# Performance work log

Measured on AMD Instinct MI355X. Metric: run time of the kernel, lower is better.

Reference implementation:

```python
import jax, jax.numpy as jnp
import numpy as np


def setup_inputs() -> dict:
    key = jax.random.key(0)
    ks = jax.random.split(key, 8)
    B, N, D, H = 8, 512, 64, 64
    user_embeddings = jax.random.normal(ks[0], (B, N, D), dtype=jnp.float32)
    past_lengths = jax.random.randint(ks[1], (B,), 0, N)
    valid_mask = jnp.ones((B, N), dtype=jnp.float32)
    # MLP params: Linear(4D -> H), PReLU (single slope), Linear(H -> 1)
    s1 = 1.0 / np.sqrt(4 * D)
    s2 = 1.0 / np.sqrt(H)
    W1 = jax.random.uniform(ks[2], (H, 4 * D), minval=-s1, maxval=s1, dtype=jnp.float32)
    b1 = jax.random.uniform(ks[3], (H,), minval=-s1, maxval=s1, dtype=jnp.float32)
    prelu_a = jnp.float32(0.25)
    W2 = jax.random.uniform(ks[4], (1, H), minval=-s2, maxval=s2, dtype=jnp.float32)
    b2 = jax.random.uniform(ks[5], (1,), minval=-s2, maxval=s2, dtype=jnp.float32)
    return {"past_lengths": past_lengths, "user_embeddings": user_embeddings,
            "valid_mask": valid_mask, "W1": W1, "b1": b1, "prelu_a": prelu_a,
            "W2": W2, "b2": b2}


def reference(past_lengths, user_embeddings, valid_mask, W1, b1, prelu_a, W2, b2):
    # DIN local activation attention with causal mask.
    # Original math: h = W1 @ concat(Q, K, Q-K, Q*K) + b1 per (q,k) pair.
    # Split W1 into its 4 D-sized blocks so the concat tensor [B,N,N,4D] is
    # never materialized; the pairwise hidden [B,N,N,H] is the only big buffer.
    B, N, D = user_embeddings.shape
    Wq, Wk, Wd, Wm = jnp.split(W1, 4, axis=1)  # each [H, D]
    x = user_embeddings
    # Q and (Q-K)'s +Q part -> per-query term; K and (Q-K)'s -K part -> per-key term
    hq = jnp.einsum('bqd,hd->bqh', x, Wq + Wd)          # [B,N,H]
    hk = jnp.einsum('bkd,hd->bkh', x, Wk - Wd)          # [B,N,H]
    hm = jnp.einsum('bqd,bkd,hd->bqkh', x, x, Wm)       # [B,N,N,H] (Q*K term)
    h = hq[:, :, None, :] + hk[:, None, :, :] + hm + b1
    h = jnp.where(h > 0, h, prelu_a * h)                # PReLU
    scores = jnp.einsum('bqkh,h->bqk', h, W2[0]) + b2[0]  # [B,N,N]
    causal = jnp.tril(jnp.ones((N, N), dtype=scores.dtype))
    scores = scores * causal[None, :, :]
    scores = scores * valid_mask[:, None, :]            # key-side padding mask
    encoded = jnp.einsum('bqk,bkd->bqd', scores, x)     # weighted sum (no softmax)
    return encoded
```

## Files before the change

kernel.cpp:

```cpp
#include <hip/hip_runtime.h>

#define NB 8
#define NN 512

#define WS_WMF 0
#define WS_HQ  4096
#define WS_BF  266240
#define WS_XE  528384

typedef float fx4 __attribute__((ext_vector_type(4)));
typedef short sx8 __attribute__((ext_vector_type(8)));
typedef int   ix4 __attribute__((ext_vector_type(4)));

static __device__ inline unsigned short f2bf(float f) {
    unsigned u = __float_as_uint(f);
    return (unsigned short)((u + 0x7FFFu + ((u >> 16) & 1u)) >> 16);
}

__global__ __launch_bounds__(256) void prep(const float* __restrict__ x,
                                            const float* __restrict__ vm,
                                            const float* __restrict__ W1,
                                            const float* __restrict__ b1,
                                            float* __restrict__ ws) {
    __shared__ float lwq[64 * 68];
    __shared__ float lwk[64 * 68];
    __shared__ float xs[256];
    const int t = threadIdx.x;
    const int blk = blockIdx.x;

    {
        int d = t & 63, hb = t >> 6;
        #pragma unroll 4
        for (int i = 0; i < 16; ++i) {
            int h = i * 4 + hb;
            float a = W1[h * 256 + d];
            float bb = W1[h * 256 + 64 + d];
            float c = W1[h * 256 + 128 + d];
            lwq[h * 68 + d] = a + c;
            lwk[h * 68 + d] = bb - c;
        }
    }
    const int r0 = blk * 4;
    xs[t] = x[r0 * 64 + t];
    __syncthreads();

    {
        int r = t >> 6, h = t & 63;
        const fx4* xr  = (const fx4*)(xs + r * 64);
        const fx4* wqv = (const fx4*)(lwq + h * 68);
        const fx4* wkv = (const fx4*)(lwk + h * 68);
        float aq = b1[h], ak = 0.f;
        #pragma unroll
        for (int dd = 0; dd < 16; ++dd) {
            fx4 xv = xr[dd];
            fx4 wq = wqv[dd];
            fx4 wk = wkv[dd];
            aq = fmaf(xv[0], wq[0], aq); aq = fmaf(xv[1], wq[1], aq);
            aq = fmaf(xv[2], wq[2], aq); aq = fmaf(xv[3], wq[3], aq);
            ak = fmaf(xv[0], wk[0], ak); ak = fmaf(xv[1], wk[1], ak);
            ak = fmaf(xv[2], wk[2], ak); ak = fmaf(xv[3], wk[3], ak);
        }
        int row = r0 + r;
        (ws + WS_HQ)[row * 64 + h] = aq;
        unsigned short* bfp = (unsigned short*)(ws + WS_BF);
        int bb = row >> 9, k = row & 511;
        int tt = k >> 4, nn = k & 15;
        int c = 2 + (h >> 5);
        int qd = (h >> 3) & 3, j = h & 7;
        int ln = qd * 16 + nn;
        bfp[((((bb * 32 + tt) * 4 + c) * 64 + ln) << 3) + j] = f2bf(ak);
    }

    if (blk < 256) {
        int b = blk >> 5, t5 = blk & 31;
        if (t < 128) {
            unsigned short* bfp = (unsigned short*)(ws + WS_BF);
            int c = t >> 6, L = t & 63;
            int nn = L & 15, qd = L >> 4;
            const float* src = x + ((b * 512 + t5 * 16 + nn) * 64 + c * 32 + qd * 8);
            fx4 v0 = *(const fx4*)src;
            fx4 v1 = *(const fx4*)(src + 4);
            uint4 o;
            o.x = (unsigned)f2bf(v0[0]) | ((unsigned)f2bf(v0[1]) << 16);
            o.y = (unsigned)f2bf(v0[2]) | ((unsigned)f2bf(v0[3]) << 16);
            o.z = (unsigned)f2bf(v1[0]) | ((unsigned)f2bf(v1[1]) << 16);
            o.w = (unsigned)f2bf(v1[2]) | ((unsigned)f2bf(v1[3]) << 16);
            *(uint4*)(bfp + ((((b * 32 + t5) * 4 + c) * 64 + L) << 3)) = o;
        }
        {
            unsigned short* xep = (unsigned short*)(ws + WS_XE);
            int c32 = t5 >> 1, half = t5 & 1;
            int nt = t >> 6, r = t & 63;
            int L = half * 32 + (r & 31);
            int j0 = (r >> 5) * 4;
            int quad = L >> 4, nn = L & 15;
            unsigned short u[4];
            #pragma unroll
            for (int i = 0; i < 4; ++i) {
                int key = c32 * 32 + quad * 8 + j0 + i;
                float v = x[(b * 512 + key) * 64 + nt * 16 + nn] * vm[b * 512 + key];
                u[i] = f2bf(v);
            }
            uint2 o;
            o.x = (unsigned)u[0] | ((unsigned)u[1] << 16);
            o.y = (unsigned)u[2] | ((unsigned)u[3] << 16);
            *(uint2*)(xep + (((((b * 16 + c32) * 4 + nt) * 64 + L) << 3) + j0)) = o;
        }
    } else if (blk < 258) {
        float* wmf = ws + WS_WMF;
        int e = (blk - 256) * 256 + t;
        int slot = e >> 6, lane = e & 63;
        int ht = slot >> 1, hf = slot & 1;
        int mm = lane & 15, qd = lane >> 4;
        int h = ht * 16 + mm;
        int dbase = hf * 32 + qd * 8;
        #pragma unroll
        for (int j = 0; j < 8; ++j)
            wmf[e * 8 + j] = W1[h * 256 + 192 + dbase + j];
    }
}

__global__ __launch_bounds__(256, 2) void k2_main(const float* __restrict__ x,
                                                  const float* __restrict__ prelu_a,
                                                  const float* __restrict__ W2,
                                                  const float* __restrict__ b2,
                                                  const float* __restrict__ ws,
                                                  float* __restrict__ out) {
    const int tid  = threadIdx.x;
    const int lane = tid & 63;
    const int w    = tid >> 6;
    const int blk  = blockIdx.x;
    const int b    = blk >> 6;
    const int rest = blk & 63;
    const int m    = rest >> 3;
    const int s    = rest & 7;
    const int n    = lane & 15, quad = lane >> 4;
    const int RA   = (m + 2) >> 1;

    const float* wmf = ws + WS_WMF;
    const float* hq  = ws + WS_HQ;
    const unsigned short* bfp = (const unsigned short*)(ws + WS_BF);
    const unsigned short* xep = (const unsigned short*)(ws + WS_XE);

    const float pa  = prelu_a[0];
    const float b2v = b2[0];

    __shared__ uint4 bufS[2][2][512];
    __shared__ uint4 bufE[2][2][256];
    __shared__ unsigned strip[4][2][16];

    fx4 w2v[4];
    #pragma unroll
    for (int ht = 0; ht < 4; ++ht)
        w2v[ht] = *(const fx4*)(W2 + ht * 16 + quad * 4);
    sx8 oh[4];
    #pragma unroll
    for (int ht = 0; ht < 4; ++ht) {
        sx8 a;
        #pragma unroll
        for (int jj = 0; jj < 8; ++jj) {
            int hp = (ht >> 1) * 32 + quad * 8 + jj;
            a[jj] = (hp == ht * 16 + n) ? (short)0x3F80 : (short)0;
        }
        oh[ht] = a;
    }
    const unsigned sel = (quad < 2) ? 0x05040100u : 0x07060302u;

    {
        int c1i = (m >= 1) ? 1 : 0;
        const uint4* sS0 = (const uint4*)(bfp + (unsigned)(b * 32) * 2048);
        const uint4* sS1 = (const uint4*)(bfp + (unsigned)(b * 32 + 2 * c1i) * 2048);
        bufS[0][0][tid] = sS0[tid]; bufS[0][0][tid + 256] = sS0[tid + 256];
        bufS[0][1][tid] = sS1[tid]; bufS[0][1][tid + 256] = sS1[tid + 256];
        bufE[0][0][tid] = ((const uint4*)(xep + (unsigned)(b * 16) * 2048))[tid];
        bufE[0][1][tid] = ((const uint4*)(xep + (unsigned)(b * 16 + c1i) * 2048))[tid];
    }
    __syncthreads();

    int r = 0;
    #pragma unroll 1
    for (int ph = 0; ph < 2; ++ph) {
        const int band   = ph ? (15 - m) : m;
        const int q      = band * 32 + s * 4 + w;
        const int bq     = b * 512 + q;
        const int rounds = ph ? (9 - RA) : RA;

        fx4 hqv[4];
        #pragma unroll
        for (int ht = 0; ht < 4; ++ht)
            hqv[ht] = *(const fx4*)(hq + bq * 64 + ht * 16 + quad * 4);
        float xq[2][8];
        {
            const float* xp = x + bq * 64 + quad * 8;
            fx4 t0 = *(const fx4*)xp;
            fx4 t1 = *(const fx4*)(xp + 4);
            fx4 t2 = *(const fx4*)(xp + 32);
            fx4 t3 = *(const fx4*)(xp + 36);
            #pragma unroll
            for (int jj = 0; jj < 4; ++jj) {
                xq[0][jj] = t0[jj]; xq[0][4 + jj] = t1[jj];
                xq[1][jj] = t2[jj]; xq[1][4 + jj] = t3[jj];
            }
        }
        sx8 afrag[4][2];
        #pragma unroll
        for (int ht = 0; ht < 4; ++ht)
            #pragma unroll
            for (int hf = 0; hf < 2; ++hf) {
                const float* wp = wmf + (((ht * 2 + hf) * 64 + lane) << 3);
                fx4 w0 = *(const fx4*)wp;
                fx4 w1 = *(const fx4*)(wp + 4);
                sx8 a;
                #pragma unroll
                for (int jj = 0; jj < 4; ++jj) {
                    a[jj]     = (short)f2bf(w0[jj] * xq[hf][jj]);
                    a[4 + jj] = (short)f2bf(w1[jj] * xq[hf][4 + jj]);
                }
                afrag[ht][hf] = a;
            }

        fx4 eacc[4];
        #pragma unroll
        for (int nt = 0; nt < 4; ++nt) eacc[nt] = (fx4){0.f, 0.f, 0.f, 0.f};

        auto do_chunk = [&](int c, int sub, int parity) {
            const unsigned short* ls = (const unsigned short*)&bufS[parity][sub][0] + lane * 8;
            sx8 fa0 = *(const sx8*)(ls);
            sx8 fa1 = *(const sx8*)(ls + 512);
            sx8 fa2 = *(const sx8*)(ls + 1024);
            sx8 fa3 = *(const sx8*)(ls + 1536);
            sx8 fb0 = *(const sx8*)(ls + 2048);
            sx8 fb1 = *(const sx8*)(ls + 2560);
            sx8 fb2 = *(const sx8*)(ls + 3072);
            sx8 fb3 = *(const sx8*)(ls + 3584);

            fx4 accA[4], accB[4];
            #pragma unroll
            for (int ht = 0; ht < 4; ++ht) { accA[ht] = hqv[ht]; accB[ht] = hqv[ht]; }
            #pragma unroll
            for (int ht = 0; ht < 4; ++ht) {
                accA[ht] = __builtin_amdgcn_mfma_f32_16x16x32_bf16(afrag[ht][0], fa0, accA[ht], 0, 0, 0);
                accB[ht] = __builtin_amdgcn_mfma_f32_16x16x32_bf16(afrag[ht][0], fb0, accB[ht], 0, 0, 0);
            }
            #pragma unroll
            for (int ht = 0; ht < 4; ++ht) {
                accA[ht] = __builtin_amdgcn_mfma_f32_16x16x32_bf16(afrag[ht][1], fa1, accA[ht], 0, 0, 0);
                accB[ht] = __builtin_amdgcn_mfma_f32_16x16x32_bf16(afrag[ht][1], fb1, accB[ht], 0, 0, 0);
            }
            #pragma unroll
            for (int ht = 0; ht < 4; ++ht) {
                accA[ht] = __builtin_amdgcn_mfma_f32_16x16x32_bf16(oh[ht], (ht < 2) ? fa2 : fa3, accA[ht], 0, 0, 0);
                accB[ht] = __builtin_amdgcn_mfma_f32_16x16x32_bf16(oh[ht], (ht < 2) ? fb2 : fb3, accB[ht], 0, 0, 0);
            }

            fx4 s0v = (fx4){0.f, 0.f, 0.f, 0.f};
            fx4 s1v = (fx4){0.f, 0.f, 0.f, 0.f};
            #pragma unroll
            for (int ht = 0; ht < 4; ++ht) {
                fx4 za = accA[ht], zb = accB[ht];
                fx4 ta = __builtin_elementwise_max(za, za * pa);
                fx4 tb = __builtin_elementwise_max(zb, zb * pa);
                s0v = ta * w2v[ht] + s0v;
                s1v = tb * w2v[ht] + s1v;
            }
            float s0 = (s0v[0] + s0v[1]) + (s0v[2] + s0v[3]);
            float s1 = (s1v[0] + s1v[1]) + (s1v[2] + s1v[3]);
            s0 += __shfl_xor(s0, 16, 64);
            s0 += __shfl_xor(s0, 32, 64);
            s1 += __shfl_xor(s1, 16, 64);
            s1 += __shfl_xor(s1, 32, 64);
            int k0 = c * 32 + n;
            s0 = (k0 <= q)      ? s0 + b2v : 0.f;
            s1 = (k0 + 16 <= q) ? s1 + b2v : 0.f;

            unsigned packed = (unsigned)f2bf(s0) | ((unsigned)f2bf(s1) << 16);
            if (quad == 0) strip[w][sub][n] = packed;
            const unsigned* sp = &strip[w][sub][(quad & 1) * 8];
            uint4 wv0 = *(const uint4*)sp;
            uint4 wv1 = *(const uint4*)(sp + 4);
            ix4 sw_;
            sw_[0] = (int)__builtin_amdgcn_perm(wv0.y, wv0.x, sel);
            sw_[1] = (int)__builtin_amdgcn_perm(wv0.w, wv0.z, sel);
            sw_[2] = (int)__builtin_amdgcn_perm(wv1.y, wv1.x, sel);
            sw_[3] = (int)__builtin_amdgcn_perm(wv1.w, wv1.z, sel);
            sx8 sfrag = __builtin_bit_cast(sx8, sw_);

            const unsigned short* le = (const unsigned short*)&bufE[parity][sub][0] + lane * 8;
            sx8 e0 = *(const sx8*)(le);
            sx8 e1 = *(const sx8*)(le + 512);
            sx8 e2 = *(const sx8*)(le + 1024);
            sx8 e3 = *(const sx8*)(le + 1536);

            eacc[0] = __builtin_amdgcn_mfma_f32_16x16x32_bf16(sfrag, e0, eacc[0], 0, 0, 0);
            eacc[1] = __builtin_amdgcn_mfma_f32_16x16x32_bf16(sfrag, e1, eacc[1], 0, 0, 0);
            eacc[2] = __builtin_amdgcn_mfma_f32_16x16x32_bf16(sfrag, e2, eacc[2], 0, 0, 0);
            eacc[3] = __builtin_amdgcn_mfma_f32_16x16x32_bf16(sfrag, e3, eacc[3], 0, 0, 0);
        };

        #pragma unroll 1
        for (int i = 0; i < rounds; ++i, ++r) {
            uint4 st0, st1, st2, st3, stE0, stE1;
            if (r < 8) {
                int nr = r + 1, c0n, c1n;
                if (nr < RA) {
                    c0n = 2 * nr; c1n = (2 * nr + 1 <= m) ? 2 * nr + 1 : m;
                } else {
                    int jj = nr - RA, cb = 15 - m;
                    c0n = 2 * jj; c1n = (2 * jj + 1 <= cb) ? 2 * jj + 1 : cb;
                }
                const uint4* sS0 = (const uint4*)(bfp + (unsigned)(b * 32 + 2 * c0n) * 2048);
                const uint4* sS1 = (const uint4*)(bfp + (unsigned)(b * 32 + 2 * c1n) * 2048);
                st0 = sS0[tid]; st1 = sS0[tid + 256];
                st2 = sS1[tid]; st3 = sS1[tid + 256];
                stE0 = ((const uint4*)(xep + (unsigned)(b * 16 + c0n) * 2048))[tid];
                stE1 = ((const uint4*)(xep + (unsigned)(b * 16 + c1n) * 2048))[tid];
            }

            do_chunk(2 * i, 0, r & 1);
            if (2 * i + 1 <= band) do_chunk(2 * i + 1, 1, r & 1);

            if (r < 8) {
                int p2 = (r + 1) & 1;
                bufS[p2][0][tid] = st0; bufS[p2][0][tid + 256] = st1;
                bufS[p2][1][tid] = st2; bufS[p2][1][tid + 256] = st3;
                bufE[p2][0][tid] = stE0; bufE[p2][1][tid] = stE1;
            }
            __syncthreads();
        }

        float ov = eacc[0][0];
        if (quad == 1) ov = eacc[1][0];
        if (quad == 2) ov = eacc[2][0];
        if (quad == 3) ov = eacc[3][0];
        out[bq * 64 + lane] = ov;
    }
}

extern "C" void kernel_launch(void* const* d_in, const int* in_sizes, int n_in,
                              void* d_out, int out_size, void* d_ws, size_t ws_size,
                              hipStream_t stream) {
    const float* x   = (const float*)d_in[1];
    const float* vmk = (const float*)d_in[2];
    const float* W1  = (const float*)d_in[3];
    const float* b1  = (const float*)d_in[4];
    const float* pa  = (const float*)d_in[5];
    const float* W2  = (const float*)d_in[6];
    const float* b2  = (const float*)d_in[7];
    float* ws  = (float*)d_ws;
    float* out = (float*)d_out;

    hipLaunchKernelGGL(prep, dim3(NB * NN / 4), dim3(256), 0, stream,
                       x, vmk, W1, b1, ws);
    hipLaunchKernelGGL(k2_main, dim3(NB * 64), dim3(256), 0, stream,
                       x, pa, W2, b2, ws, out);
}
```

Before: 102.6 us.

## Replace paired-band load balancing with one band per block, heaviest bands first

The main kernel previously gave each block two complementary causal bands (m and 15-m) so every block did equal work across 512 blocks. Now each of 1024 blocks handles a single 32-query band, with blocks ordered so the longest bands launch first, and processes one 32-key chunk per iteration with a smaller double buffer. This halves shared memory per block and doubles the block count to raise occupancy and parallelism. The cost is uneven per-block work, more barrier iterations per chunk, and redundant setup (afrag, hq loads) per block.

```diff
diff --git a/kernel.cpp b/kernel.cpp
--- a/kernel.cpp
+++ b/kernel.cpp
@@ -130,12 +130,14 @@
     const int lane = tid & 63;
     const int w    = tid >> 6;
     const int blk  = blockIdx.x;
-    const int b    = blk >> 6;
+    const int band = 15 - (blk >> 6);
     const int rest = blk & 63;
-    const int m    = rest >> 3;
+    const int b    = rest >> 3;
     const int s    = rest & 7;
     const int n    = lane & 15, quad = lane >> 4;
-    const int RA   = (m + 2) >> 1;
+    const int q    = band * 32 + s * 4 + w;
+    const int bq   = b * 512 + q;
+    const int cmax = band;
 
     const float* wmf = ws + WS_WMF;
     const float* hq  = ws + WS_HQ;
@@ -145,9 +147,9 @@
     const float pa  = prelu_a[0];
     const float b2v = b2[0];
 
-    __shared__ uint4 bufS[2][2][512];
-    __shared__ uint4 bufE[2][2][256];
-    __shared__ unsigned strip[4][2][16];
+    __shared__ uint4 bufS[2][512];
+    __shared__ uint4 bufE[2][256];
+    __shared__ unsigned strip[4][16];
 
     fx4 w2v[4];
     #pragma unroll
@@ -166,174 +168,149 @@
     }
     const unsigned sel = (quad < 2) ? 0x05040100u : 0x07060302u;
 
+    fx4 hqv[4];
+    #pragma unroll
+    for (int ht = 0; ht < 4; ++ht)
+        hqv[ht] = *(const fx4*)(hq + bq * 64 + ht * 16 + quad * 4);
+    float xq[2][8];
     {
-        int c1i = (m >= 1) ? 1 : 0;
-        const uint4* sS0 = (const uint4*)(bfp + (unsigned)(b * 32) * 2048);
-        const uint4* sS1 = (const uint4*)(bfp + (unsigned)(b * 32 + 2 * c1i) * 2048);
-        bufS[0][0][tid] = sS0[tid]; bufS[0][0][tid + 256] = sS0[tid + 256];
-        bufS[0][1][tid] = sS1[tid]; bufS[0][1][tid + 256] = sS1[tid + 256];
-        bufE[0][0][tid] = ((const uint4*)(xep + (unsigned)(b * 16) * 2048))[tid];
-        bufE[0][1][tid] = ((const uint4*)(xep + (unsigned)(b * 16 + c1i) * 2048))[tid];
-    }
-    __syncthreads();
-
-    int r = 0;
-    #pragma unroll 1
-    for (int ph = 0; ph < 2; ++ph) {
-        const int band   = ph ? (15 - m) : m;
-        const int q      = band * 32 + s * 4 + w;
-        const int bq     = b * 512 + q;
-        const int rounds = ph ? (9 - RA) : RA;
-
-        fx4 hqv[4];
-        #pragma unroll
-        for (int ht = 0; ht < 4; ++ht)
-            hqv[ht] = *(const fx4*)(hq + bq * 64 + ht * 16 + quad * 4);
-        float xq[2][8];
-        {
-            const float* xp = x + bq * 64 + quad * 8;
-            fx4 t0 = *(const fx4*)xp;
-            fx4 t1 = *(const fx4*)(xp + 4);
-            fx4 t2 = *(const fx4*)(xp + 32);
-            fx4 t3 = *(const fx4*)(xp + 36);
+        const float* xp = x + bq * 64 + quad * 8;
+        fx4 t0 = *(const fx4*)xp;
+        fx4 t1 = *(const fx4*)(xp + 4);
+        fx4 t2 = *(const fx4*)(xp + 32);
+        fx4 t3 = *(const fx4*)(xp + 36);
+        #pragma unroll
+        for (int jj = 0; jj < 4; ++jj) {
+            xq[0][jj] = t0[jj]; xq[0][4 + jj] = t1[jj];
+            xq[1][jj] = t2[jj]; xq[1][4 + jj] = t3[jj];
+        }
+    }
+    sx8 afrag[4][2];
+    #pragma unroll
+    for (int ht = 0; ht < 4; ++ht)
+        #pragma unroll
+        for (int hf = 0; hf < 2; ++hf) {
+            const float* wp = wmf + (((ht * 2 + hf) * 64 + lane) << 3);
+            fx4 w0 = *(const fx4*)wp;
+            fx4 w1 = *(const fx4*)(wp + 4);
+            sx8 a;
             #pragma unroll
             for (int jj = 0; jj < 4; ++jj) {
-                xq[0][jj] = t0[jj]; xq[0][4 + jj] = t1[jj];
-                xq[1][jj] = t2[jj]; xq[1][4 + jj] = t3[jj];
+                a[jj]     = (short)f2bf(w0[jj] * xq[hf][jj]);
+                a[4 + jj] = (short)f2bf(w1[jj] * xq[hf][4 + jj]);
             }
-        }
-        sx8 afrag[4][2];
-        #pragma unroll
-        for (int ht = 0; ht < 4; ++ht)
-            #pragma unroll
-            for (int hf = 0; hf < 2; ++hf) {
-                const float* wp = wmf + (((ht * 2 + hf) * 64 + lane) << 3);
-                fx4 w0 = *(const fx4*)wp;
-                fx4 w1 = *(const fx4*)(wp + 4);
-                sx8 a;
-                #pragma unroll
-                for (int jj = 0; jj < 4; ++jj) {
-                    a[jj]     = (short)f2bf(w0[jj] * xq[hf][jj]);
-                    a[4 + jj] = (short)f2bf(w1[jj] * xq[hf][4 + jj]);
-                }
-                afrag[ht][hf] = a;
-            }
-
-        fx4 eacc[4];
-        #pragma unroll
-        for (int nt = 0; nt < 4; ++nt) eacc[nt] = (fx4){0.f, 0.f, 0.f, 0.f};
-
-        auto do_chunk = [&](int c, int sub, int parity) {
-            const unsigned short* ls = (const unsigned short*)&bufS[parity][sub][0] + lane * 8;
-            sx8 fa0 = *(const sx8*)(ls);
-            sx8 fa1 = *(const sx8*)(ls + 512);
-            sx8 fa2 = *(const sx8*)(ls + 1024);
-            sx8 fa3 = *(const sx8*)(ls + 1536);
-            sx8 fb0 = *(const sx8*)(ls + 2048);
-            sx8 fb1 = *(const sx8*)(ls + 2560);
-            sx8 fb2 = *(const sx8*)(ls + 3072);
-            sx8 fb3 = *(const sx8*)(ls + 3584);
-
-            fx4 accA[4], accB[4];
-            #pragma unroll
-            for (int ht = 0; ht < 4; ++ht) { accA[ht] = hqv[ht]; accB[ht] = hqv[ht]; }
-            #pragma unroll
-            for (int ht = 0; ht < 4; ++ht) {
-                accA[ht] = __builtin_amdgcn_mfma_f32_16x16x32_bf16(afrag[ht][0], fa0, accA[ht], 0, 0, 0);
-                accB[ht] = __builtin_amdgcn_mfma_f32_16x16x32_bf16(afrag[ht][0], fb0, accB[ht], 0, 0, 0);
-            }
-            #pragma unroll
-            for (int ht = 0; ht < 4; ++ht) {
-                accA[ht] = __builtin_amdgcn_mfma_f32_16x16x32_bf16(afrag[ht][1], fa1, accA[ht], 0, 0, 0);
-                accB[ht] = __builtin_amdgcn_mfma_f32_16x16x32_bf16(afrag[ht][1], fb1, accB[ht], 0, 0, 0);
-            }
-            #pragma unroll
-            for (int ht = 0; ht < 4; ++ht) {
-                accA[ht] = __builtin_amdgcn_mfma_f32_16x16x32_bf16(oh[ht], (ht < 2) ? fa2 : fa3, accA[ht], 0, 0, 0);
-                accB[ht] = __builtin_amdgcn_mfma_f32_16x16x32_bf16(oh[ht], (ht < 2) ? fb2 : fb3, accB[ht], 0, 0, 0);
-            }
-
-            fx4 s0v = (fx4){0.f, 0.f, 0.f, 0.f};
-            fx4 s1v = (fx4){0.f, 0.f, 0.f, 0.f};
-            #pragma unroll
-            for (int ht = 0; ht < 4; ++ht) {
-                fx4 za = accA[ht], zb = accB[ht];
-                fx4 ta = __builtin_elementwise_max(za, za * pa);
-                fx4 tb = __builtin_elementwise_max(zb, zb * pa);
-                s0v = ta * w2v[ht] + s0v;
-                s1v = tb * w2v[ht] + s1v;
-            }
-            float s0 = (s0v[0] + s0v[1]) + (s0v[2] + s0v[3]);
-            float s1 = (s1v[0] + s1v[1]) + (s1v[2] + s1v[3]);
-            s0 += __shfl_xor(s0, 16, 64);
-            s0 += __shfl_xor(s0, 32, 64);
-            s1 += __shfl_xor(s1, 16, 64);
-            s1 += __shfl_xor(s1, 32, 64);
-            int k0 = c * 32 + n;
-            s0 = (k0 <= q)      ? s0 + b2v : 0.f;
-            s1 = (k0 + 16 <= q) ? s1 + b2v : 0.f;
-
-            unsigned packed = (unsigned)f2bf(s0) | ((unsigned)f2bf(s1) << 16);
-            if (quad == 0) strip[w][sub][n] = packed;
-            const unsigned* sp = &strip[w][sub][(quad & 1) * 8];
-            uint4 wv0 = *(const uint4*)sp;
-            uint4 wv1 = *(const uint4*)(sp + 4);
-            ix4 sw_;
-            sw_[0] = (int)__builtin_amdgcn_perm(wv0.y, wv0.x, sel);
-            sw_[1] = (int)__builtin_amdgcn_perm(wv0.w, wv0.z, sel);
-            sw_[2] = (int)__builtin_amdgcn_perm(wv1.y, wv1.x, sel);
-            sw_[3] = (int)__builtin_amdgcn_perm(wv1.w, wv1.z, sel);
-            sx8 sfrag = __builtin_bit_cast(sx8, sw_);
-
-            const unsigned short* le = (const unsigned short*)&bufE[parity][sub][0] + lane * 8;
-            sx8 e0 = *(const sx8*)(le);
-            sx8 e1 = *(const sx8*)(le + 512);
-            sx8 e2 = *(const sx8*)(le + 1024);
-            sx8 e3 = *(const sx8*)(le + 1536);
-
-            eacc[0] = __builtin_amdgcn_mfma_f32_16x16x32_bf16(sfrag, e0, eacc[0], 0, 0, 0);
-            eacc[1] = __builtin_amdgcn_mfma_f32_16x16x32_bf16(sfrag, e1, eacc[1], 0, 0, 0);
-            eacc[2] = __builtin_amdgcn_mfma_f32_16x16x32_bf16(sfrag, e2, eacc[2], 0, 0, 0);
-            eacc[3] = __builtin_amdgcn_mfma_f32_16x16x32_bf16(sfrag, e3, eacc[3], 0, 0, 0);
-        };
-
-        #pragma unroll 1
-        for (int i = 0; i < rounds; ++i, ++r) {
-            uint4 st0, st1, st2, st3, stE0, stE1;
-            if (r < 8) {
-                int nr = r + 1, c0n, c1n;
-                if (nr < RA) {
-                    c0n = 2 * nr; c1n = (2 * nr + 1 <= m) ? 2 * nr + 1 : m;
-                } else {
-                    int jj = nr - RA, cb = 15 - m;
-                    c0n = 2 * jj; c1n = (2 * jj + 1 <= cb) ? 2 * jj + 1 : cb;
-                }
-                const uint4* sS0 = (const uint4*)(bfp + (unsigned)(b * 32 + 2 * c0n) * 2048);
-                const uint4* sS1 = (const uint4*)(bfp + (unsigned)(b * 32 + 2 * c1n) * 2048);
-                st0 = sS0[tid]; st1 = sS0[tid + 256];
-                st2 = sS1[tid]; st3 = sS1[tid + 256];
-                stE0 = ((const uint4*)(xep + (unsigned)(b * 16 + c0n) * 2048))[tid];
-                stE1 = ((const uint4*)(xep + (unsigned)(b * 16 + c1n) * 2048))[tid];
-            }
-
-            do_chunk(2 * i, 0, r & 1);
-            if (2 * i + 1 <= band) do_chunk(2 * i + 1, 1, r & 1);
-
-            if (r < 8) {
-                int p2 = (r + 1) & 1;
-                bufS[p2][0][tid] = st0; bufS[p2][0][tid + 256] = st1;
-                bufS[p2][1][tid] = st2; bufS[p2][1][tid + 256] = st3;
-                bufE[p2][0][tid] = stE0; bufE[p2][1][tid] = stE1;
-            }
-            __syncthreads();
-        }
-
-        float ov = eacc[0][0];
-        if (quad == 1) ov = eacc[1][0];
-        if (quad == 2) ov = eacc[2][0];
-        if (quad == 3) ov = eacc[3][0];
-        out[bq * 64 + lane] = ov;
-    }
+            afrag[ht][hf] = a;
+        }
+
+    fx4 eacc[4];
+    #pragma unroll
+    for (int nt = 0; nt < 4; ++nt) eacc[nt] = (fx4){0.f, 0.f, 0.f, 0.f};
+
+    {
+        const uint4* sS = (const uint4*)(bfp + (unsigned)(b * 32) * 2048);
+        bufS[0][tid]       = sS[tid];
+        bufS[0][tid + 256] = sS[tid + 256];
+        bufE[0][tid] = ((const uint4*)(xep + (unsigned)(b * 16) * 2048))[tid];
+    }
+    __syncthreads();
+
+    #pragma unroll 1
+    for (int c = 0; c <= cmax; ++c) {
+        uint4 st0, st1, stE;
+        if (c < cmax) {
+            const uint4* sS = (const uint4*)(bfp + (unsigned)(b * 32 + 2 * (c + 1)) * 2048);
+            st0 = sS[tid];
+            st1 = sS[tid + 256];
+            stE = ((const uint4*)(xep + (unsigned)(b * 16 + c + 1) * 2048))[tid];
+        }
+
+        const int p = c & 1;
+        const unsigned short* ls = (const unsigned short*)&bufS[p][0] + lane * 8;
+        sx8 fa0 = *(const sx8*)(ls);
+        sx8 fa1 = *(const sx8*)(ls + 512);
+        sx8 fa2 = *(const sx8*)(ls + 1024);
+        sx8 fa3 = *(const sx8*)(ls + 1536);
+        sx8 fb0 = *(const sx8*)(ls + 2048);
+        sx8 fb1 = *(const sx8*)(ls + 2560);
+        sx8 fb2 = *(const sx8*)(ls + 3072);
+        sx8 fb3 = *(const sx8*)(ls + 3584);
+
+        fx4 accA[4], accB[4];
+        #pragma unroll
+        for (int ht = 0; ht < 4; ++ht) { accA[ht] = hqv[ht]; accB[ht] = hqv[ht]; }
+        #pragma unroll
+        for (int ht = 0; ht < 4; ++ht) {
+            accA[ht] = __builtin_amdgcn_mfma_f32_16x16x32_bf16(afrag[ht][0], fa0, accA[ht], 0, 0, 0);
+            accB[ht] = __builtin_amdgcn_mfma_f32_16x16x32_bf16(afrag[ht][0], fb0, accB[ht], 0, 0, 0);
+        }
+        #pragma unroll
+        for (int ht = 0; ht < 4; ++ht) {
+            accA[ht] = __builtin_amdgcn_mfma_f32_16x16x32_bf16(afrag[ht][1], fa1, accA[ht], 0, 0, 0);
+            accB[ht] = __builtin_amdgcn_mfma_f32_16x16x32_bf16(afrag[ht][1], fb1, accB[ht], 0, 0, 0);
+        }
+        #pragma unroll
+        for (int ht = 0; ht < 4; ++ht) {
+            accA[ht] = __builtin_amdgcn_mfma_f32_16x16x32_bf16(oh[ht], (ht < 2) ? fa2 : fa3, accA[ht], 0, 0, 0);
+            accB[ht] = __builtin_amdgcn_mfma_f32_16x16x32_bf16(oh[ht], (ht < 2) ? fb2 : fb3, accB[ht], 0, 0, 0);
+        }
+
+        fx4 s0v = (fx4){0.f, 0.f, 0.f, 0.f};
+        fx4 s1v = (fx4){0.f, 0.f, 0.f, 0.f};
+        #pragma unroll
+        for (int ht = 0; ht < 4; ++ht) {
+            fx4 za = accA[ht], zb = accB[ht];
+            fx4 ta = __builtin_elementwise_max(za, za * pa);
+            fx4 tb = __builtin_elementwise_max(zb, zb * pa);
+            s0v = ta * w2v[ht] + s0v;
+            s1v = tb * w2v[ht] + s1v;
+        }
+        float s0 = (s0v[0] + s0v[1]) + (s0v[2] + s0v[3]);
+        float s1 = (s1v[0] + s1v[1]) + (s1v[2] + s1v[3]);
+        s0 += __shfl_xor(s0, 16, 64);
+        s0 += __shfl_xor(s0, 32, 64);
+        s1 += __shfl_xor(s1, 16, 64);
+        s1 += __shfl_xor(s1, 32, 64);
+        int k0 = c * 32 + n;
+        s0 = (k0 <= q)      ? s0 + b2v : 0.f;
+        s1 = (k0 + 16 <= q) ? s1 + b2v : 0.f;
+
+        unsigned packed = (unsigned)f2bf(s0) | ((unsigned)f2bf(s1) << 16);
+        if (quad == 0) strip[w][n] = packed;
+        const unsigned* sp = &strip[w][(quad & 1) * 8];
+        uint4 wv0 = *(const uint4*)sp;
+        uint4 wv1 = *(const uint4*)(sp + 4);
+        ix4 sw_;
+        sw_[0] = (int)__builtin_amdgcn_perm(wv0.y, wv0.x, sel);
+        sw_[1] = (int)__builtin_amdgcn_perm(wv0.w, wv0.z, sel);
+        sw_[2] = (int)__builtin_amdgcn_perm(wv1.y, wv1.x, sel);
+        sw_[3] = (int)__builtin_amdgcn_perm(wv1.w, wv1.z, sel);
+        sx8 sfrag = __builtin_bit_cast(sx8, sw_);
+
+        const unsigned short* le = (const unsigned short*)&bufE[p][0] + lane * 8;
+        sx8 e0 = *(const sx8*)(le);
+        sx8 e1 = *(const sx8*)(le + 512);
+        sx8 e2 = *(const sx8*)(le + 1024);
+        sx8 e3 = *(const sx8*)(le + 1536);
+
+        eacc[0] = __builtin_amdgcn_mfma_f32_16x16x32_bf16(sfrag, e0, eacc[0], 0, 0, 0);
+        eacc[1] = __builtin_amdgcn_mfma_f32_16x16x32_bf16(sfrag, e1, eacc[1], 0, 0, 0);
+        eacc[2] = __builtin_amdgcn_mfma_f32_16x16x32_bf16(sfrag, e2, eacc[2], 0, 0, 0);
+        eacc[3] = __builtin_amdgcn_mfma_f32_16x16x32_bf16(sfrag, e3, eacc[3], 0, 0, 0);
+
+        if (c < cmax) {
+            const int p2 = (c + 1) & 1;
+            bufS[p2][tid]       = st0;
+            bufS[p2][tid + 256] = st1;
+            bufE[p2][tid]       = stE;
+        }
+        __syncthreads();
+    }
+
+    float ov = eacc[0][0];
+    if (quad == 1) ov = eacc[1][0];
+    if (quad == 2) ov = eacc[2][0];
+    if (quad == 3) ov = eacc[3][0];
+    out[bq * 64 + lane] = ov;
 }
 
 extern "C" void kernel_launch(void* const* d_in, const int* in_sizes, int n_in,
@@ -351,6 +328,6 @@
 
     hipLaunchKernelGGL(prep, dim3(NB * NN / 4), dim3(256), 0, stream,
                        x, vmk, W1, b1, ws);
-    hipLaunchKernelGGL(k2_main, dim3(NB * 64), dim3(256), 0, stream,
+    hipLaunchKernelGGL(k2_main, dim3(1024), dim3(256), 0, stream,
                        x, pa, W2, b2, ws, out);
 }
```

Result: faster. 99.26 us (-3.2%).
